# Kernel tuning notes

Hardware: AMD Instinct MI355X
Metric: run time of the kernel (lower is better)

Reference implementation:

```python
import jax, jax.numpy as jnp
import numpy as np
from jax import lax

BS, H, W, NA = 128, 64, 64, 4
C1, C2, HID = 16, 32, 512

def setup_inputs() -> dict:
    key = jax.random.key(0)
    ks = jax.random.split(key, 12)
    s = 0.05
    return {
        "diffs": jax.random.uniform(ks[0], (BS, NA, 2), jnp.float32) * 4.0,  # agent locations
        "states": jax.random.normal(ks[1], (BS, NA * 3, H, W), jnp.float32),
        "conv1_w": jax.random.normal(ks[2], (C1, 3, 8, 8), jnp.float32) * s,
        "conv1_b": jnp.zeros((C1,), jnp.float32),
        "conv2_w": jax.random.normal(ks[3], (C2, C1, 5, 5), jnp.float32) * s,
        "conv2_b": jnp.zeros((C2,), jnp.float32),
        "g_w": jax.random.normal(ks[4], (HID, 2 * C2 + 2), jnp.float32) * s,
        "g_b": jnp.zeros((HID,), jnp.float32),
        "fc4_w": jax.random.normal(ks[5], (2, HID), jnp.float32) * s,
        "fc4_b": jnp.zeros((2,), jnp.float32),
        "fc5_w": jax.random.normal(ks[6], (1, HID), jnp.float32) * s,
        "fc5_b": jnp.zeros((1,), jnp.float32),
    }

def _conv(x, w, b):
    y = lax.conv_general_dilated(x, w, (1, 1), 'VALID',
                                 dimension_numbers=('NCHW', 'OIHW', 'NCHW'))
    return jax.nn.relu(y + b[None, :, None, None])

def reference(diffs, states, conv1_w, conv1_b, conv2_w, conv2_b,
              g_w, g_b, fc4_w, fc4_b, fc5_w, fc5_b):
    bs = states.shape[0]
    # ---- encoder: per-agent CNN + global max pool ----
    x = states.reshape(bs * NA, 3, H, W)
    x = _conv(x, conv1_w, conv1_b)
    x = _conv(x, conv2_w, conv2_b)
    feat = jnp.max(x, axis=(2, 3)).reshape(bs, NA, C2)  # (bs, 4, 32)
    # ---- coordinator: adjacency from pairwise location diffs ----
    locs = diffs
    pdiffs = locs[:, :, None, :] - locs[:, None, :, :]  # (bs, 4, 4, 2)
    norms = jnp.linalg.norm(pdiffs, axis=-1)
    thresh = jnp.linalg.norm(jnp.array([1.0, 1.0], jnp.float32))
    A = (norms < thresh).astype(jnp.float32)
    A = A / jnp.clip(jnp.sum(A, axis=-1, keepdims=True), 1e-6)  # row-normalized adjacency
    mask = 1.0 - jnp.eye(NA, dtype=jnp.float32)  # messages skip j == i
    Am = A * mask  # (bs, 4, 4)
    # ---- CatEdgeGraphLayer: h_i = relu(W [f_i ; sum_j A_ij [f_j ; d_ij]] + b) ----
    feat_agg = jnp.einsum('bij,bjc->bic', Am, feat)          # (bs, 4, 32)
    diff_agg = jnp.einsum('bij,bijd->bid', Am, pdiffs)       # (bs, 4, 2)
    h = jnp.concatenate([feat, feat_agg, diff_agg], axis=-1)  # (bs, 4, 66)
    h = jax.nn.relu(jnp.einsum('bic,oc->bio', h, g_w) + g_b)  # (bs, 4, 512)
    policies = jnp.einsum('bic,oc->bio', h, fc4_w) + fc4_b    # (bs, 4, 2)
    values = jnp.einsum('bic,oc->bio', h, fc5_w) + fc5_b      # (bs, 4, 1)
    return (policies, values)
```

## Files before the change

kernel.cpp:

```cpp
#include <hip/hip_runtime.h>
#include <hip/hip_bf16.h>

#define H1 57
#define H2 53
#define XP 60

typedef _Float16 f16;
typedef _Float16 f16x4 __attribute__((ext_vector_type(4)));
typedef _Float16 f16x8 __attribute__((ext_vector_type(8)));
typedef float f32x4 __attribute__((ext_vector_type(4)));
typedef float f32x16 __attribute__((ext_vector_type(16)));

__global__ __launch_bounds__(256) void k_repack(const float* __restrict__ w1,
    const float* __restrict__ w2, const float* __restrict__ gw,
    f16* __restrict__ w1f, f16* __restrict__ w2f,
    float2* __restrict__ gwT2, float* __restrict__ feat)
{
  const int tid = blockIdx.x * 256 + threadIdx.x;
  const int stride = 32 * 256;
  for (int i = tid; i < 8 * 64 * 8; i += stride) {
    int j = i & 7;
    int l = (i >> 3) & 63;
    int tp = i >> 9;
    int c = j & 3;
    int kw = 2 * (l >> 4) + (j >> 2);
    int oc = l & 15;
    float v = (c < 3) ? w1[((oc * 3 + c) * 8 + tp) * 8 + kw] : 0.f;
    w1f[i] = (f16)v;
  }
  for (int i = tid; i < 25 * 64 * 8; i += stride) {
    int j = i & 7;
    int l = (i >> 3) & 63;
    int tap = i >> 9;
    int oc = l & 31;
    int ch = ((l >> 5) << 3) + j;
    w2f[i] = (f16)w2[((oc * 16 + ch) * 5 + tap / 5) * 5 + tap % 5];
  }
  for (int i = tid; i < 66 * 256; i += stride) {
    int t = i & 255;
    int c = i >> 8;
    float2 v;
    v.x = gw[(2 * t) * 66 + c];
    v.y = gw[(2 * t + 1) * 66 + c];
    gwT2[i] = v;
  }
  for (int i = tid; i < 512 * 32; i += stride) feat[i] = 0.f;
}

__global__ __launch_bounds__(256) void k_conv1(const float* __restrict__ in,
    const f16* __restrict__ w1f, const float* __restrict__ b1,
    f16* __restrict__ O1)
{
  __shared__ __align__(16) f16 sIn[15][72][4];
  __shared__ __align__(16) f16 sT[4][64][20];
  const int img = blockIdx.x;
  const int y0 = min((int)blockIdx.y * 8, 49);
  const int lane = threadIdx.x & 63;
  const int wv = threadIdx.x >> 6;

  f16x8 Bf[8];
  #pragma unroll
  for (int tp = 0; tp < 8; ++tp)
    Bf[tp] = *(const f16x8*)&w1f[(tp * 64 + lane) * 8];

  for (int i = threadIdx.x; i < 15 * 16; i += 256) {
    int y = i >> 4, xq = i & 15;
    const float* p0 = &in[(((size_t)img * 3 + 0) * 64 + (y0 + y)) * 64 + xq * 4];
    float4 v0 = *(const float4*)p0;
    float4 v1 = *(const float4*)(p0 + 4096);
    float4 v2 = *(const float4*)(p0 + 8192);
    float c0[4] = {v0.x, v0.y, v0.z, v0.w};
    float c1[4] = {v1.x, v1.y, v1.z, v1.w};
    float c2[4] = {v2.x, v2.y, v2.z, v2.w};
    #pragma unroll
    for (int q = 0; q < 4; ++q) {
      f16x4 tt = {(f16)c0[q], (f16)c1[q], (f16)c2[q], (f16)0.f};
      *(f16x4*)&sIn[y][xq * 4 + q][0] = tt;
    }
  }
  for (int i = threadIdx.x; i < 15 * 8; i += 256) {
    int y = i >> 3, xi = i & 7;
    *(f16x4*)&sIn[y][64 + xi][0] = (f16x4){(f16)0.f, (f16)0.f, (f16)0.f, (f16)0.f};
  }
  __syncthreads();

  const int g = lane >> 4;
  const int n16 = lane & 15;

  const float bias = b1[n16];
  f32x4 acc[2][4];
  #pragma unroll
  for (int r = 0; r < 2; ++r)
    #pragma unroll
    for (int xt = 0; xt < 4; ++xt)
      acc[r][xt] = (f32x4){bias, bias, bias, bias};

  #pragma unroll
  for (int tp = 0; tp < 8; ++tp) {
    #pragma unroll
    for (int r = 0; r < 2; ++r) {
      const int row = 2 * wv + r + tp;
      #pragma unroll
      for (int xt = 0; xt < 4; ++xt) {
        const int px = xt * 16 + n16;
        f16x4 a0 = *(const f16x4*)&sIn[row][px + 2 * g][0];
        f16x4 a1 = *(const f16x4*)&sIn[row][px + 2 * g + 1][0];
        union { struct { f16x4 lo, hi; } pr; f16x8 v; } u;
        u.pr.lo = a0; u.pr.hi = a1;
        acc[r][xt] = __builtin_amdgcn_mfma_f32_16x16x32_f16(u.v, Bf[tp], acc[r][xt], 0, 0, 0);
      }
    }
  }

  #pragma unroll
  for (int r = 0; r < 2; ++r) {
    #pragma unroll
    for (int xt = 0; xt < 4; ++xt)
      #pragma unroll
      for (int q = 0; q < 4; ++q)
        sT[wv][xt * 16 + g * 4 + q][n16] = (f16)fmaxf(acc[r][xt][q], 0.f);
    const int yy = y0 + 2 * wv + r;
    if (lane < H1) {
      f16x4 v0 = *(const f16x4*)&sT[wv][lane][0];
      f16x4 v1 = *(const f16x4*)&sT[wv][lane][4];
      f16x4 v2 = *(const f16x4*)&sT[wv][lane][8];
      f16x4 v3 = *(const f16x4*)&sT[wv][lane][12];
      union { struct { f16x4 a, b; } pr; f16x8 v; } lo, hi;
      lo.pr.a = v0; lo.pr.b = v1;
      hi.pr.a = v2; hi.pr.b = v3;
      f16* dst = &O1[((((size_t)img * H1 + yy) * 2 + 0) * XP + lane) * 8];
      *(f16x8*)dst = lo.v;
      *(f16x8*)(dst + XP * 8) = hi.v;
    }
  }
}

__global__ __launch_bounds__(256, 4) void k_conv2(const f16* __restrict__ O1,
    const f16* __restrict__ w2f, const float* __restrict__ b2,
    float* __restrict__ feat)
{
  __shared__ __align__(16) f16 sW[17 * 64 * 8];
  __shared__ __align__(16) f16 sI[12 * 2 * XP * 8 + 64];
  __shared__ unsigned smax[32];
  const int img = blockIdx.x;
  const int y0 = min((int)blockIdx.y * 8, 45);
  const int lane = threadIdx.x & 63;
  const int wv = threadIdx.x >> 6;
  if (threadIdx.x < 32) smax[threadIdx.x] = 0u;

  f16x8 Br[8];
  const f16* pBg = &w2f[lane * 8];
  #pragma unroll
  for (int t = 0; t < 8; ++t)
    Br[t] = *(const f16x8*)(pBg + t * 512);

  for (int i = threadIdx.x; i < 17 * 64; i += 256)
    ((float4*)sW)[i] = ((const float4*)w2f)[8 * 64 + i];
  {
    const float4* src = (const float4*)(O1 + (size_t)(img * H1 + y0) * (2 * XP * 8));
    for (int i = threadIdx.x; i < 1440; i += 256)
      ((float4*)sI)[i] = src[i];
  }
  __syncthreads();

  const int m32 = lane & 31;
  const int G = lane >> 5;

  const int start = (wv < 2) ? wv * 4 : 8 + (wv - 2) * 3;
  const int cnt = (wv < 2) ? 4 : 3;

  const float bias = b2[m32];
  f32x16 acc[4];
  #pragma unroll
  for (int ti = 0; ti < 4; ++ti)
    #pragma unroll
    for (int q = 0; q < 16; ++q)
      acc[ti][q] = bias;

  const f16* pA[4];
  #pragma unroll
  for (int ti = 0; ti < 4; ++ti) {
    int t = start + ti;
    int p = t * 32 + m32;
    p = min(p, 423);
    int y = (p * 1237) >> 16;
    int x = p - 53 * y;
    pA[ti] = &sI[((y * 2 + G) * XP + x) * 8];
  }

  #pragma unroll
  for (int tap = 0; tap < 25; ++tap) {
    const int kh = tap / 5, kw = tap % 5;
    const int off = (kh * 2 * XP + kw) * 8;
    f16x8 Bv = (tap < 8) ? Br[tap] : *(const f16x8*)(&sW[lane * 8] + (tap - 8) * 512);
    #pragma unroll
    for (int ti = 0; ti < 4; ++ti) {
      if (ti < cnt) {
        f16x8 Av = *(const f16x8*)(pA[ti] + off);
        acc[ti] = __builtin_amdgcn_mfma_f32_32x32x16_f16(Av, Bv, acc[ti], 0, 0, 0);
      }
    }
  }

  float m = 0.f;
  #pragma unroll
  for (int ti = 0; ti < 4; ++ti) {
    if (ti < cnt) {
      const int t = start + ti;
      #pragma unroll
      for (int q = 0; q < 16; ++q) {
        if (t == 13 && q >= 4) continue;
        m = fmaxf(m, acc[ti][q]);
      }
    }
  }
  m = fmaxf(m, 0.f);
  m = fmaxf(m, __shfl_xor(m, 32, 64));
  if (lane < 32) atomicMax(&smax[m32], __float_as_uint(m));
  __syncthreads();
  if (threadIdx.x < 32)
    atomicMax((unsigned*)&feat[img * 32 + threadIdx.x], smax[threadIdx.x]);
}

__global__ __launch_bounds__(256) void k_head(const float* __restrict__ diffs,
    const float* __restrict__ feat, const float2* __restrict__ gwT2,
    const float* __restrict__ gb, const float* __restrict__ w4,
    const float* __restrict__ b4, const float* __restrict__ w5,
    const float* __restrict__ b5, float* __restrict__ out)
{
  __shared__ float h66[4][66];
  __shared__ float hout[4][512];
  __shared__ float Am[4][4];
  __shared__ float pd[4][4][2];
  __shared__ float fs[4][32];
  const int b = blockIdx.x;
  const int tid = threadIdx.x;
  if (tid < 128) {
    int i = tid >> 5, c = tid & 31;
    fs[i][c] = feat[(b * 4 + i) * 32 + c];
  }
  if (tid == 0) {
    float lx[4], ly[4];
    #pragma unroll
    for (int a = 0; a < 4; ++a) {
      lx[a] = diffs[(b * 4 + a) * 2];
      ly[a] = diffs[(b * 4 + a) * 2 + 1];
    }
    #pragma unroll
    for (int i = 0; i < 4; ++i) {
      float A[4];
      float rs = 0.f;
      #pragma unroll
      for (int j = 0; j < 4; ++j) {
        float dx = lx[i] - lx[j], dy = ly[i] - ly[j];
        pd[i][j][0] = dx;
        pd[i][j][1] = dy;
        float n = sqrtf(dx * dx + dy * dy);
        A[j] = (n < 1.41421356237309504880f) ? 1.f : 0.f;
        rs += A[j];
      }
      float inv = 1.f / fmaxf(rs, 1e-6f);
      #pragma unroll
      for (int j = 0; j < 4; ++j)
        Am[i][j] = (i == j) ? 0.f : A[j] * inv;
    }
  }
  __syncthreads();
  if (tid < 128) {
    int i = tid >> 5, c = tid & 31;
    h66[i][c] = fs[i][c];
    float s = 0.f;
    #pragma unroll
    for (int j = 0; j < 4; ++j) s += Am[i][j] * fs[j][c];
    h66[i][32 + c] = s;
  } else if (tid < 136) {
    int q = tid - 128;
    int i = q >> 1, d = q & 1;
    float s = 0.f;
    #pragma unroll
    for (int j = 0; j < 4; ++j) s += Am[i][j] * pd[i][j][d];
    h66[i][64 + d] = s;
  }
  __syncthreads();
  {
    const float b0 = gb[2 * tid], b1g = gb[2 * tid + 1];
    float a[4][2];
    #pragma unroll
    for (int i = 0; i < 4; ++i) { a[i][0] = b0; a[i][1] = b1g; }
    #pragma unroll 6
    for (int c = 0; c < 66; ++c) {
      float2 w = gwT2[c * 256 + tid];
      #pragma unroll
      for (int i = 0; i < 4; ++i) {
        float h = h66[i][c];
        a[i][0] = fmaf(h, w.x, a[i][0]);
        a[i][1] = fmaf(h, w.y, a[i][1]);
      }
    }
    #pragma unroll
    for (int i = 0; i < 4; ++i) {
      float2 v;
      v.x = fmaxf(a[i][0], 0.f);
      v.y = fmaxf(a[i][1], 0.f);
      *(float2*)&hout[i][2 * tid] = v;
    }
  }
  __syncthreads();
  if (tid < 192) {
    int gq = tid >> 4, l = tid & 15;
    int i = gq / 3, k = gq % 3;
    const float* wrow = (k < 2) ? &w4[k * 512] : w5;
    float s = 0.f;
    for (int o = l; o < 512; o += 16) s = fmaf(hout[i][o], wrow[o], s);
    #pragma unroll
    for (int d = 8; d >= 1; d >>= 1) s += __shfl_xor(s, d, 16);
    if (l == 0) {
      if (k < 2) out[(b * 4 + i) * 2 + k] = s + b4[k];
      else       out[1024 + b * 4 + i] = s + b5[0];
    }
  }
}

extern "C" void kernel_launch(void* const* d_in, const int* in_sizes, int n_in,
                              void* d_out, int out_size, void* d_ws, size_t ws_size,
                              hipStream_t stream) {
  const float* diffs  = (const float*)d_in[0];
  const float* states = (const float*)d_in[1];
  const float* w1 = (const float*)d_in[2];
  const float* b1 = (const float*)d_in[3];
  const float* w2 = (const float*)d_in[4];
  const float* b2 = (const float*)d_in[5];
  const float* gw = (const float*)d_in[6];
  const float* gb = (const float*)d_in[7];
  const float* w4 = (const float*)d_in[8];
  const float* b4 = (const float*)d_in[9];
  const float* w5 = (const float*)d_in[10];
  const float* b5 = (const float*)d_in[11];
  float* out = (float*)d_out;

  char* base = (char*)d_ws;
  f16*    w1f  = (f16*)base;
  f16*    w2f  = (f16*)(base + 8192);
  float2* gwT2 = (float2*)(base + 34816);
  float*  feat = (float*)(base + 169984);
  f16*    O1   = (f16*)(base + 235520);

  k_repack<<<32, 256, 0, stream>>>(w1, w2, gw, w1f, w2f, gwT2, feat);
  k_conv1<<<dim3(512, 8), 256, 0, stream>>>(states, w1f, b1, O1);
  k_conv2<<<dim3(512, 7), 256, 0, stream>>>(O1, w2f, b2, feat);
  k_head<<<128, 256, 0, stream>>>(diffs, feat, gwT2, gb, w4, b4, w5, b5, out);
}
```

Before: 88.22 us.

## Drop conv1 LDS transpose via swapped MFMA operands; pad conv2 input rows

Conv1 swaps the MFMA A/B operands so each lane holds four consecutive output channels for one pixel. It then writes f16x4 directly to global memory, removing the shared-memory transpose buffer and its stores and reloads. Conv2 pads each input row in LDS to a stride of 968 halves, meant to reduce bank conflicts on the A-operand loads. It also keeps one more weight tap in registers, at the cost of more register pressure. The conv1 global writes become narrower (8-byte instead of 16-byte) and more scattered, which may hurt coalescing.

```diff
diff --git a/kernel.cpp b/kernel.cpp
--- a/kernel.cpp
+++ b/kernel.cpp
@@ -4,6 +4,7 @@
 #define H1 57
 #define H2 53
 #define XP 60
+#define SIP 968
 
 typedef _Float16 f16;
 typedef _Float16 f16x4 __attribute__((ext_vector_type(4)));
@@ -52,7 +53,6 @@
     f16* __restrict__ O1)
 {
   __shared__ __align__(16) f16 sIn[15][72][4];
-  __shared__ __align__(16) f16 sT[4][64][20];
   const int img = blockIdx.x;
   const int y0 = min((int)blockIdx.y * 8, 49);
   const int lane = threadIdx.x & 63;
@@ -87,13 +87,13 @@
   const int g = lane >> 4;
   const int n16 = lane & 15;
 
-  const float bias = b1[n16];
+  const f32x4 biasv = {b1[g * 4 + 0], b1[g * 4 + 1], b1[g * 4 + 2], b1[g * 4 + 3]};
   f32x4 acc[2][4];
   #pragma unroll
   for (int r = 0; r < 2; ++r)
     #pragma unroll
     for (int xt = 0; xt < 4; ++xt)
-      acc[r][xt] = (f32x4){bias, bias, bias, bias};
+      acc[r][xt] = biasv;
 
   #pragma unroll
   for (int tp = 0; tp < 8; ++tp) {
@@ -107,30 +107,24 @@
         f16x4 a1 = *(const f16x4*)&sIn[row][px + 2 * g + 1][0];
         union { struct { f16x4 lo, hi; } pr; f16x8 v; } u;
         u.pr.lo = a0; u.pr.hi = a1;
-        acc[r][xt] = __builtin_amdgcn_mfma_f32_16x16x32_f16(u.v, Bf[tp], acc[r][xt], 0, 0, 0);
+        acc[r][xt] = __builtin_amdgcn_mfma_f32_16x16x32_f16(Bf[tp], u.v, acc[r][xt], 0, 0, 0);
       }
     }
   }
 
   #pragma unroll
   for (int r = 0; r < 2; ++r) {
-    #pragma unroll
-    for (int xt = 0; xt < 4; ++xt)
-      #pragma unroll
-      for (int q = 0; q < 4; ++q)
-        sT[wv][xt * 16 + g * 4 + q][n16] = (f16)fmaxf(acc[r][xt][q], 0.f);
     const int yy = y0 + 2 * wv + r;
-    if (lane < H1) {
-      f16x4 v0 = *(const f16x4*)&sT[wv][lane][0];
-      f16x4 v1 = *(const f16x4*)&sT[wv][lane][4];
-      f16x4 v2 = *(const f16x4*)&sT[wv][lane][8];
-      f16x4 v3 = *(const f16x4*)&sT[wv][lane][12];
-      union { struct { f16x4 a, b; } pr; f16x8 v; } lo, hi;
-      lo.pr.a = v0; lo.pr.b = v1;
-      hi.pr.a = v2; hi.pr.b = v3;
-      f16* dst = &O1[((((size_t)img * H1 + yy) * 2 + 0) * XP + lane) * 8];
-      *(f16x8*)dst = lo.v;
-      *(f16x8*)(dst + XP * 8) = hi.v;
+    f16* rowp = &O1[(((size_t)img * H1 + yy) * 2 + (g >> 1)) * XP * 8 + (g & 1) * 4];
+    #pragma unroll
+    for (int xt = 0; xt < 4; ++xt) {
+      const int px = xt * 16 + n16;
+      if (px < H1) {
+        f16x4 v;
+        #pragma unroll
+        for (int q = 0; q < 4; ++q) v[q] = (f16)fmaxf(acc[r][xt][q], 0.f);
+        *(f16x4*)&rowp[px * 8] = v;
+      }
     }
   }
 }
@@ -139,8 +133,8 @@
     const f16* __restrict__ w2f, const float* __restrict__ b2,
     float* __restrict__ feat)
 {
-  __shared__ __align__(16) f16 sW[17 * 64 * 8];
-  __shared__ __align__(16) f16 sI[12 * 2 * XP * 8 + 64];
+  __shared__ __align__(16) f16 sW[16 * 64 * 8];
+  __shared__ __align__(16) f16 sI[12 * SIP + 16];
   __shared__ unsigned smax[32];
   const int img = blockIdx.x;
   const int y0 = min((int)blockIdx.y * 8, 45);
@@ -148,18 +142,21 @@
   const int wv = threadIdx.x >> 6;
   if (threadIdx.x < 32) smax[threadIdx.x] = 0u;
 
-  f16x8 Br[8];
+  f16x8 Br[9];
   const f16* pBg = &w2f[lane * 8];
   #pragma unroll
-  for (int t = 0; t < 8; ++t)
+  for (int t = 0; t < 9; ++t)
     Br[t] = *(const f16x8*)(pBg + t * 512);
 
-  for (int i = threadIdx.x; i < 17 * 64; i += 256)
-    ((float4*)sW)[i] = ((const float4*)w2f)[8 * 64 + i];
+  for (int i = threadIdx.x; i < 16 * 64; i += 256)
+    ((float4*)sW)[i] = ((const float4*)w2f)[9 * 64 + i];
   {
     const float4* src = (const float4*)(O1 + (size_t)(img * H1 + y0) * (2 * XP * 8));
-    for (int i = threadIdx.x; i < 1440; i += 256)
-      ((float4*)sI)[i] = src[i];
+    for (int i = threadIdx.x; i < 1440; i += 256) {
+      int y = i / 120;
+      int rem = i - y * 120;
+      ((float4*)&sI[y * SIP])[rem] = src[i];
+    }
   }
   __syncthreads();
 
@@ -185,14 +182,14 @@
     p = min(p, 423);
     int y = (p * 1237) >> 16;
     int x = p - 53 * y;
-    pA[ti] = &sI[((y * 2 + G) * XP + x) * 8];
+    pA[ti] = &sI[y * SIP + G * 480 + x * 8];
   }
 
   #pragma unroll
   for (int tap = 0; tap < 25; ++tap) {
     const int kh = tap / 5, kw = tap % 5;
-    const int off = (kh * 2 * XP + kw) * 8;
-    f16x8 Bv = (tap < 8) ? Br[tap] : *(const f16x8*)(&sW[lane * 8] + (tap - 8) * 512);
+    const int off = kh * SIP + kw * 8;
+    f16x8 Bv = (tap < 9) ? Br[tap] : *(const f16x8*)(&sW[lane * 8] + (tap - 9) * 512);
     #pragma unroll
     for (int ti = 0; ti < 4; ++ti) {
       if (ti < cnt) {
```

New measurement: 86.84 us. No clear change (-1.6%).
